# Optimization experiments

Hardware: AMD Instinct MI355X
Metric: run time of the kernel (lower is better)

## Reference

```python
import jax, jax.numpy as jnp
import numpy as np

D_MODEL = 1024
N_HEADS = 16
HEAD_DIM = D_MODEL // N_HEADS
D_FF = 4096
BATCH = 128
MEM_LEN = 1024
LN_EPS = 1e-5


def _layernorm(x, gamma, beta):
    mu = jnp.mean(x, axis=-1, keepdims=True)
    var = jnp.mean(jnp.square(x - mu), axis=-1, keepdims=True)
    return (x - mu) * jax.lax.rsqrt(var + LN_EPS) * gamma + beta


def setup_inputs() -> dict:
    key = jax.random.key(0)
    ks = jax.random.split(key, 12)
    s = 0.02
    return {
        "x": jax.random.normal(ks[0], (BATCH, D_MODEL), jnp.float32),
        "memory_keys": jax.random.normal(ks[1], (BATCH, MEM_LEN, D_MODEL), jnp.float32),
        "memory_values": jax.random.normal(ks[2], (BATCH, MEM_LEN, D_MODEL), jnp.float32),
        "alibi_bias": jax.random.normal(ks[3], (N_HEADS, 1, MEM_LEN), jnp.float32),
        "Wq": jax.random.normal(ks[4], (D_MODEL, D_MODEL), jnp.float32) * s,
        "bq": jnp.zeros((D_MODEL,), jnp.float32),
        "Wo": jax.random.normal(ks[5], (D_MODEL, D_MODEL), jnp.float32) * s,
        "bo": jnp.zeros((D_MODEL,), jnp.float32),
        "W1": jax.random.normal(ks[6], (D_MODEL, D_FF), jnp.float32) * s,
        "b1": jnp.zeros((D_FF,), jnp.float32),
        "W2": jax.random.normal(ks[7], (D_FF, D_MODEL), jnp.float32) * s,
        "b2": jnp.zeros((D_MODEL,), jnp.float32),
        "g1": jnp.ones((D_MODEL,), jnp.float32),
        "be1": jnp.zeros((D_MODEL,), jnp.float32),
        "g2": jnp.ones((D_MODEL,), jnp.float32),
        "be2": jnp.zeros((D_MODEL,), jnp.float32),
    }


def reference(x, memory_keys, memory_values, alibi_bias,
              Wq, bq, Wo, bo, W1, b1, W2, b2, g1, be1, g2, be2):
    B = x.shape[0]
    M = memory_keys.shape[1]
    # Q projection for the single query position: (B, H, hd)
    q = (x @ Wq + bq).reshape(B, N_HEADS, HEAD_DIM)
    k = memory_keys.reshape(B, M, N_HEADS, HEAD_DIM)
    v = memory_values.reshape(B, M, N_HEADS, HEAD_DIM)
    scale = 1.0 / np.sqrt(HEAD_DIM).astype(np.float32)
    # scores: (B, H, M) = q . k + ALiBi bias (broadcast over batch)
    scores = jnp.einsum("bhd,bmhd->bhm", q, k) * scale + alibi_bias[:, 0, :][None]
    attn = jax.nn.softmax(scores, axis=-1)
    attn_out = jnp.einsum("bhm,bmhd->bhd", attn, v).reshape(B, D_MODEL)
    attn_out = attn_out @ Wo + bo
    # residual + norm1 (dropout disabled in eval mode)
    h = _layernorm(x + attn_out, g1, be1)
    ff = jax.nn.relu(h @ W1 + b1) @ W2 + b2
    return _layernorm(h + ff, g2, be2)
```

## Files before the change

kernel.cpp:

```cpp
#include <hip/hip_runtime.h>
#include <hip/hip_bf16.h>
#include <math.h>

#define BATCH   128
#define DMODEL  1024
#define NHEADS  16
#define HEADDIM 64
#define DFF     4096
#define MEMLEN  1024
#define SPLIT   8
#define CHUNK   (MEMLEN / SPLIT)
#define QSPLIT  8
#define F1SPLIT 4
#define F2SPLIT 16

typedef __attribute__((ext_vector_type(8))) __bf16 bf16x8;
typedef __attribute__((ext_vector_type(4))) __bf16 bf16x4;
typedef __attribute__((ext_vector_type(4))) float  f32x4;

template<int ABF16, int KCHUNK>
__global__ __launch_bounds__(256) void gemm_k(
    const float* __restrict__ Af, const __bf16* __restrict__ Ab,
    const float* __restrict__ W, const float* __restrict__ bias,
    float* __restrict__ C, int N, int K)
{
    const int t    = threadIdx.x;
    const int lane = t & 63;
    const int w    = t >> 6;
    const int n0   = blockIdx.x * 64;
    const int m0   = blockIdx.y * 64;
    const int z    = blockIdx.z;
    const int kbeg = z * KCHUNK;

    __shared__ __bf16 As[2][64 * 56];
    __shared__ __bf16 Bs[2][64 * 56];

    const int ar = t >> 2, ac = (t & 3) * 8;
    const int bn = t & 63, bk = w * 8;
    const int q = lane >> 4, l15 = lane & 15;
    constexpr int ITERS = KCHUNK / 32;

    f32x4 acc[4] = {f32x4{0,0,0,0}, f32x4{0,0,0,0}, f32x4{0,0,0,0}, f32x4{0,0,0,0}};

    const float* wB   = W + (size_t)(kbeg + bk) * N + n0 + bn;
    const size_t aOff = (size_t)(m0 + ar) * K + kbeg + ac;

    {
        bf16x8 av;
        if constexpr (ABF16) {
            av = *(const bf16x8*)(Ab + aOff);
        } else {
            const float* ap = Af + aOff;
            float4 a0 = *(const float4*)ap, a1 = *(const float4*)(ap + 4);
            av[0]=(__bf16)a0.x; av[1]=(__bf16)a0.y; av[2]=(__bf16)a0.z; av[3]=(__bf16)a0.w;
            av[4]=(__bf16)a1.x; av[5]=(__bf16)a1.y; av[6]=(__bf16)a1.z; av[7]=(__bf16)a1.w;
        }
        bf16x8 bv;
        #pragma unroll
        for (int j = 0; j < 8; j++) bv[j] = (__bf16)wB[(size_t)j * N];
        *(bf16x8*)&As[0][ar * 56 + ac] = av;
        *(bf16x8*)&Bs[0][bn * 56 + bk] = bv;
    }
    __syncthreads();

    int cur = 0;
    #pragma unroll
    for (int it = 1; it < ITERS; ++it) {
        bf16x8 avn;
        float ax[8];
        if constexpr (ABF16) {
            avn = *(const bf16x8*)(Ab + aOff + it * 32);
        } else {
            const float* ap = Af + aOff + it * 32;
            float4 a0 = *(const float4*)ap, a1 = *(const float4*)(ap + 4);
            ax[0]=a0.x; ax[1]=a0.y; ax[2]=a0.z; ax[3]=a0.w;
            ax[4]=a1.x; ax[5]=a1.y; ax[6]=a1.z; ax[7]=a1.w;
        }
        float br[8];
        const float* wp = wB + (size_t)(it * 32) * N;
        #pragma unroll
        for (int j = 0; j < 8; j++) br[j] = wp[(size_t)j * N];

        bf16x8 af = *(const bf16x8*)&As[cur][(w * 16 + l15) * 56 + q * 8];
        #pragma unroll
        for (int c = 0; c < 4; c++) {
            bf16x8 bfv = *(const bf16x8*)&Bs[cur][(c * 16 + l15) * 56 + q * 8];
            acc[c] = __builtin_amdgcn_mfma_f32_16x16x32_bf16(af, bfv, acc[c], 0, 0, 0);
        }

        if constexpr (!ABF16) {
            #pragma unroll
            for (int j = 0; j < 8; j++) avn[j] = (__bf16)ax[j];
        }
        bf16x8 bvn;
        #pragma unroll
        for (int j = 0; j < 8; j++) bvn[j] = (__bf16)br[j];
        *(bf16x8*)&As[cur ^ 1][ar * 56 + ac] = avn;
        *(bf16x8*)&Bs[cur ^ 1][bn * 56 + bk] = bvn;
        __syncthreads();
        cur ^= 1;
    }

    {
        bf16x8 af = *(const bf16x8*)&As[cur][(w * 16 + l15) * 56 + q * 8];
        #pragma unroll
        for (int c = 0; c < 4; c++) {
            bf16x8 bfv = *(const bf16x8*)&Bs[cur][(c * 16 + l15) * 56 + q * 8];
            acc[c] = __builtin_amdgcn_mfma_f32_16x16x32_bf16(af, bfv, acc[c], 0, 0, 0);
        }
    }

    float* Cp = C + (size_t)z * ((size_t)BATCH * N);
    #pragma unroll
    for (int c = 0; c < 4; c++) {
        const int col = n0 + c * 16 + l15;
        const float bb = (z == 0) ? bias[col] : 0.0f;
        #pragma unroll
        for (int r = 0; r < 4; r++) {
            const int row = m0 + w * 16 + q * 4 + r;
            Cp[(size_t)row * N + col] = acc[c][r] + bb;
        }
    }
}

__global__ __launch_bounds__(256) void qsum_k(
    const float* __restrict__ qpart, float* __restrict__ qsum)
{
    const int b = blockIdx.x;
    const int t = threadIdx.x;
    const size_t idx = (size_t)b * DMODEL + 4 * t;
    float4 a = {0.f, 0.f, 0.f, 0.f};
    #pragma unroll
    for (int z = 0; z < QSPLIT; z++) {
        const float4 v = *(const float4*)&qpart[(size_t)z * (BATCH * DMODEL) + idx];
        a.x += v.x; a.y += v.y; a.z += v.z; a.w += v.w;
    }
    a.x *= 0.125f; a.y *= 0.125f; a.z *= 0.125f; a.w *= 0.125f;
    *(float4*)&qsum[idx] = a;
}

__global__ __launch_bounds__(256) void attn_partial_k(
    const float* __restrict__ qsum, const float* __restrict__ Kd,
    const float* __restrict__ Vd, const float* __restrict__ alibi,
    float* __restrict__ pacc, float* __restrict__ pl)
{
    const int s = blockIdx.x;
    const int b = blockIdx.y;
    const int t = threadIdx.x;
    const int h = t >> 4;

    const float4 qv = *(const float4*)&qsum[(size_t)b * DMODEL + 4 * t];
    float  l   = 0.0f;
    f32x4  acc = {0.f, 0.f, 0.f, 0.f};

    const size_t base = (size_t)b * MEMLEN * DMODEL + 4 * t;
    const float* __restrict__ ali = alibi + (size_t)h * MEMLEN + s * CHUNK;
    const size_t off0 = base + (size_t)(s * CHUNK) * DMODEL;

    #pragma unroll 4
    for (int i = 0; i < CHUNK; i++) {
        const size_t off = off0 + (size_t)i * DMODEL;
        const float4 kv = *(const float4*)&Kd[off];
        const float4 vv = *(const float4*)&Vd[off];
        float d = kv.x * qv.x + kv.y * qv.y + kv.z * qv.z + kv.w * qv.w;
        d += __shfl_xor(d, 1);
        d += __shfl_xor(d, 2);
        d += __shfl_xor(d, 4);
        d += __shfl_xor(d, 8);
        const float pw = __expf(d + ali[i]);
        l += pw;
        acc.x += pw * vv.x;
        acc.y += pw * vv.y;
        acc.z += pw * vv.z;
        acc.w += pw * vv.w;
    }
    *(f32x4*)&pacc[((size_t)(b * SPLIT + s)) * DMODEL + 4 * t] = acc;
    if ((t & 15) == 0) pl[(b * SPLIT + s) * NHEADS + h] = l;
}

__global__ __launch_bounds__(256) void attn_combine_k(
    const float* __restrict__ pacc, const float* __restrict__ pl,
    __bf16* __restrict__ attnb)
{
    const int b = blockIdx.x;
    const int t = threadIdx.x;
    const int h = t >> 4;

    float  L   = 0.0f;
    float4 acc = {0.f, 0.f, 0.f, 0.f};
    #pragma unroll
    for (int s = 0; s < SPLIT; s++) {
        L += pl[(b * SPLIT + s) * NHEADS + h];
        const float4 pa = *(const float4*)
            &pacc[((size_t)(b * SPLIT + s)) * DMODEL + 4 * t];
        acc.x += pa.x; acc.y += pa.y; acc.z += pa.z; acc.w += pa.w;
    }
    const float inv = 1.0f / L;
    bf16x4 o;
    o[0] = (__bf16)(acc.x * inv); o[1] = (__bf16)(acc.y * inv);
    o[2] = (__bf16)(acc.z * inv); o[3] = (__bf16)(acc.w * inv);
    *(bf16x4*)&attnb[(size_t)b * DMODEL + 4 * t] = o;
}

template<int NPARTS, bool WRITE_BF16>
__global__ __launch_bounds__(256) void ln_k(
    const float* __restrict__ xres, const float* __restrict__ parts,
    const float* __restrict__ g, const float* __restrict__ be,
    float* __restrict__ of32, __bf16* __restrict__ obf)
{
    const int b = blockIdx.x;
    const int t = threadIdx.x;
    float4 sv = *(const float4*)&xres[(size_t)b * DMODEL + 4 * t];
    #pragma unroll
    for (int z = 0; z < NPARTS; z++) {
        const float4 yv = *(const float4*)
            &parts[(size_t)z * (BATCH * DMODEL) + (size_t)b * DMODEL + 4 * t];
        sv.x += yv.x; sv.y += yv.y; sv.z += yv.z; sv.w += yv.w;
    }
    float sum = sv.x + sv.y + sv.z + sv.w;
    float sq  = sv.x * sv.x + sv.y * sv.y + sv.z * sv.z + sv.w * sv.w;
    #pragma unroll
    for (int mask = 1; mask < 64; mask <<= 1) {
        sum += __shfl_xor(sum, mask);
        sq  += __shfl_xor(sq, mask);
    }
    __shared__ float red[8];
    const int w = t >> 6;
    if ((t & 63) == 0) { red[w * 2] = sum; red[w * 2 + 1] = sq; }
    __syncthreads();
    sum = red[0] + red[2] + red[4] + red[6];
    sq  = red[1] + red[3] + red[5] + red[7];

    const float mu  = sum * (1.0f / DMODEL);
    const float var = sq * (1.0f / DMODEL) - mu * mu;
    const float rs  = rsqrtf(var + 1e-5f);

    const float4 gv  = *(const float4*)&g[4 * t];
    const float4 bev = *(const float4*)&be[4 * t];
    float4 o;
    o.x = (sv.x - mu) * rs * gv.x + bev.x;
    o.y = (sv.y - mu) * rs * gv.y + bev.y;
    o.z = (sv.z - mu) * rs * gv.z + bev.z;
    o.w = (sv.w - mu) * rs * gv.w + bev.w;
    *(float4*)&of32[(size_t)b * DMODEL + 4 * t] = o;
    if constexpr (WRITE_BF16) {
        bf16x4 ob;
        ob[0] = (__bf16)o.x; ob[1] = (__bf16)o.y;
        ob[2] = (__bf16)o.z; ob[3] = (__bf16)o.w;
        *(bf16x4*)&obf[(size_t)b * DMODEL + 4 * t] = ob;
    }
}

__global__ __launch_bounds__(256) void ff1reduce_k(
    const float* __restrict__ ffbpart, __bf16* __restrict__ ff1act)
{
    const int t = threadIdx.x;
    const size_t base = (size_t)blockIdx.x * 2048 + t * 8;
    float4 s0 = {0.f, 0.f, 0.f, 0.f}, s1 = {0.f, 0.f, 0.f, 0.f};
    #pragma unroll
    for (int z = 0; z < F1SPLIT; z++) {
        const float* pp = ffbpart + (size_t)z * ((size_t)BATCH * DFF) + base;
        const float4 a  = *(const float4*)pp;
        const float4 b4 = *(const float4*)(pp + 4);
        s0.x += a.x;  s0.y += a.y;  s0.z += a.z;  s0.w += a.w;
        s1.x += b4.x; s1.y += b4.y; s1.z += b4.z; s1.w += b4.w;
    }
    bf16x8 o;
    o[0] = (__bf16)fmaxf(s0.x, 0.f); o[1] = (__bf16)fmaxf(s0.y, 0.f);
    o[2] = (__bf16)fmaxf(s0.z, 0.f); o[3] = (__bf16)fmaxf(s0.w, 0.f);
    o[4] = (__bf16)fmaxf(s1.x, 0.f); o[5] = (__bf16)fmaxf(s1.y, 0.f);
    o[6] = (__bf16)fmaxf(s1.z, 0.f); o[7] = (__bf16)fmaxf(s1.w, 0.f);
    *(bf16x8*)&ff1act[base] = o;
}

extern "C" void kernel_launch(void* const* d_in, const int* in_sizes, int n_in,
                              void* d_out, int out_size, void* d_ws, size_t ws_size,
                              hipStream_t stream)
{
    const float* x   = (const float*)d_in[0];
    const float* mk  = (const float*)d_in[1];
    const float* mv  = (const float*)d_in[2];
    const float* ab  = (const float*)d_in[3];
    const float* Wq  = (const float*)d_in[4];
    const float* bq  = (const float*)d_in[5];
    const float* Wo  = (const float*)d_in[6];
    const float* bo  = (const float*)d_in[7];
    const float* W1  = (const float*)d_in[8];
    const float* b1  = (const float*)d_in[9];
    const float* W2  = (const float*)d_in[10];
    const float* b2  = (const float*)d_in[11];
    const float* g1  = (const float*)d_in[12];
    const float* be1 = (const float*)d_in[13];
    const float* g2  = (const float*)d_in[14];
    const float* be2 = (const float*)d_in[15];
    float* out = (float*)d_out;

    float* wsf      = (float*)d_ws;
    float* qpart    = wsf;
    float* qsum     = wsf + 1048576;
    float* tmppart  = wsf + 1179648;
    float* hbuf     = wsf + 2228224;
    float* ffbpart  = wsf + 2359296;
    float* tmp2part = wsf + 4456448;
    float* pacc     = wsf + 6553600;
    float* pl       = wsf + 7602176;
    __bf16* attnb   = (__bf16*)(wsf + 7618560);
    __bf16* hbf     = (__bf16*)(wsf + 7684096);
    __bf16* ff1act  = (__bf16*)(wsf + 7749632);

    gemm_k<0, DMODEL / QSPLIT><<<dim3(16, 2, QSPLIT), 256, 0, stream>>>(
        x, nullptr, Wq, bq, qpart, DMODEL, DMODEL);
    qsum_k<<<BATCH, 256, 0, stream>>>(qpart, qsum);
    attn_partial_k<<<dim3(SPLIT, BATCH), 256, 0, stream>>>(
        qsum, mk, mv, ab, pacc, pl);
    attn_combine_k<<<BATCH, 256, 0, stream>>>(pacc, pl, attnb);
    gemm_k<1, DMODEL / QSPLIT><<<dim3(16, 2, QSPLIT), 256, 0, stream>>>(
        nullptr, attnb, Wo, bo, tmppart, DMODEL, DMODEL);
    ln_k<QSPLIT, true><<<BATCH, 256, 0, stream>>>(
        x, tmppart, g1, be1, hbuf, hbf);
    gemm_k<1, DMODEL / F1SPLIT><<<dim3(64, 2, F1SPLIT), 256, 0, stream>>>(
        nullptr, hbf, W1, b1, ffbpart, DFF, DMODEL);
    ff1reduce_k<<<(BATCH * DFF) / 2048, 256, 0, stream>>>(ffbpart, ff1act);
    gemm_k<1, DFF / F2SPLIT><<<dim3(16, 2, F2SPLIT), 256, 0, stream>>>(
        nullptr, ff1act, W2, b2, tmp2part, DMODEL, DFF);
    ln_k<F2SPLIT, false><<<BATCH, 256, 0, stream>>>(
        hbuf, tmp2part, g2, be2, out, nullptr);
}
```

Baseline: 1.055 ms.

## Fuse split-K reductions into consumer kernels and retune split factors

Removes the separate qsum and ff1reduce kernels. The attention partial kernel now sums the Q split-K partials itself, and the W2 GEMM sums two FF1 partials and applies ReLU while loading its A operand. Split factors are retuned: attention memory split doubled, and the Q, FF1 and FF2 K-splits halved. The GEMM loop count becomes a runtime value instead of a compile-time unrolled constant, which may cost some scheduling quality. Each attention block re-reads the Q partials redundantly, and FF2 reads fp32 inputs instead of bf16.

After: 1.071 ms. Within noise of the previous version (+1.5%).

```diff
diff --git a/kernel.cpp b/kernel.cpp
--- a/kernel.cpp
+++ b/kernel.cpp
@@ -8,21 +8,22 @@
 #define HEADDIM 64
 #define DFF     4096
 #define MEMLEN  1024
-#define SPLIT   8
+#define SPLIT   16
 #define CHUNK   (MEMLEN / SPLIT)
-#define QSPLIT  8
-#define F1SPLIT 4
-#define F2SPLIT 16
+#define QSPLIT  4
+#define F1SPLIT 2
+#define F2SPLIT 8
 
 typedef __attribute__((ext_vector_type(8))) __bf16 bf16x8;
 typedef __attribute__((ext_vector_type(4))) __bf16 bf16x4;
 typedef __attribute__((ext_vector_type(4))) float  f32x4;
 
-template<int ABF16, int KCHUNK>
+template<int ABF16, int APARTS, int RELU>
 __global__ __launch_bounds__(256) void gemm_k(
-    const float* __restrict__ Af, const __bf16* __restrict__ Ab,
+    const float* __restrict__ Af, size_t aPartStride,
+    const __bf16* __restrict__ Ab,
     const float* __restrict__ W, const float* __restrict__ bias,
-    float* __restrict__ C, int N, int K)
+    float* __restrict__ C, int N, int K, int kchunk)
 {
     const int t    = threadIdx.x;
     const int lane = t & 63;
@@ -30,7 +31,7 @@
     const int n0   = blockIdx.x * 64;
     const int m0   = blockIdx.y * 64;
     const int z    = blockIdx.z;
-    const int kbeg = z * KCHUNK;
+    const int kbeg = z * kchunk;
 
     __shared__ __bf16 As[2][64 * 56];
     __shared__ __bf16 Bs[2][64 * 56];
@@ -38,7 +39,6 @@
     const int ar = t >> 2, ac = (t & 3) * 8;
     const int bn = t & 63, bk = w * 8;
     const int q = lane >> 4, l15 = lane & 15;
-    constexpr int ITERS = KCHUNK / 32;
 
     f32x4 acc[4] = {f32x4{0,0,0,0}, f32x4{0,0,0,0}, f32x4{0,0,0,0}, f32x4{0,0,0,0}};
 
@@ -52,8 +52,19 @@
         } else {
             const float* ap = Af + aOff;
             float4 a0 = *(const float4*)ap, a1 = *(const float4*)(ap + 4);
-            av[0]=(__bf16)a0.x; av[1]=(__bf16)a0.y; av[2]=(__bf16)a0.z; av[3]=(__bf16)a0.w;
-            av[4]=(__bf16)a1.x; av[5]=(__bf16)a1.y; av[6]=(__bf16)a1.z; av[7]=(__bf16)a1.w;
+            float va[8] = {a0.x, a0.y, a0.z, a0.w, a1.x, a1.y, a1.z, a1.w};
+            if constexpr (APARTS == 2) {
+                const float* a2 = ap + aPartStride;
+                float4 y0 = *(const float4*)a2, y1 = *(const float4*)(a2 + 4);
+                va[0]+=y0.x; va[1]+=y0.y; va[2]+=y0.z; va[3]+=y0.w;
+                va[4]+=y1.x; va[5]+=y1.y; va[6]+=y1.z; va[7]+=y1.w;
+            }
+            #pragma unroll
+            for (int j = 0; j < 8; j++) {
+                float v = va[j];
+                if (RELU) v = fmaxf(v, 0.0f);
+                av[j] = (__bf16)v;
+            }
         }
         bf16x8 bv;
         #pragma unroll
@@ -63,9 +74,9 @@
     }
     __syncthreads();
 
+    const int iters = kchunk >> 5;
     int cur = 0;
-    #pragma unroll
-    for (int it = 1; it < ITERS; ++it) {
+    for (int it = 1; it < iters; ++it) {
         bf16x8 avn;
         float ax[8];
         if constexpr (ABF16) {
@@ -75,6 +86,12 @@
             float4 a0 = *(const float4*)ap, a1 = *(const float4*)(ap + 4);
             ax[0]=a0.x; ax[1]=a0.y; ax[2]=a0.z; ax[3]=a0.w;
             ax[4]=a1.x; ax[5]=a1.y; ax[6]=a1.z; ax[7]=a1.w;
+            if constexpr (APARTS == 2) {
+                const float* a2 = ap + aPartStride;
+                float4 y0 = *(const float4*)a2, y1 = *(const float4*)(a2 + 4);
+                ax[0]+=y0.x; ax[1]+=y0.y; ax[2]+=y0.z; ax[3]+=y0.w;
+                ax[4]+=y1.x; ax[5]+=y1.y; ax[6]+=y1.z; ax[7]+=y1.w;
+            }
         }
         float br[8];
         const float* wp = wB + (size_t)(it * 32) * N;
@@ -90,7 +107,11 @@
 
         if constexpr (!ABF16) {
             #pragma unroll
-            for (int j = 0; j < 8; j++) avn[j] = (__bf16)ax[j];
+            for (int j = 0; j < 8; j++) {
+                float v = ax[j];
+                if (RELU) v = fmaxf(v, 0.0f);
+                avn[j] = (__bf16)v;
+            }
         }
         bf16x8 bvn;
         #pragma unroll
@@ -123,24 +144,8 @@
     }
 }
 
-__global__ __launch_bounds__(256) void qsum_k(
-    const float* __restrict__ qpart, float* __restrict__ qsum)
-{
-    const int b = blockIdx.x;
-    const int t = threadIdx.x;
-    const size_t idx = (size_t)b * DMODEL + 4 * t;
-    float4 a = {0.f, 0.f, 0.f, 0.f};
-    #pragma unroll
-    for (int z = 0; z < QSPLIT; z++) {
-        const float4 v = *(const float4*)&qpart[(size_t)z * (BATCH * DMODEL) + idx];
-        a.x += v.x; a.y += v.y; a.z += v.z; a.w += v.w;
-    }
-    a.x *= 0.125f; a.y *= 0.125f; a.z *= 0.125f; a.w *= 0.125f;
-    *(float4*)&qsum[idx] = a;
-}
-
 __global__ __launch_bounds__(256) void attn_partial_k(
-    const float* __restrict__ qsum, const float* __restrict__ Kd,
+    const float* __restrict__ qpart, const float* __restrict__ Kd,
     const float* __restrict__ Vd, const float* __restrict__ alibi,
     float* __restrict__ pacc, float* __restrict__ pl)
 {
@@ -149,7 +154,16 @@
     const int t = threadIdx.x;
     const int h = t >> 4;
 
-    const float4 qv = *(const float4*)&qsum[(size_t)b * DMODEL + 4 * t];
+    float4 qv = {0.f, 0.f, 0.f, 0.f};
+    #pragma unroll
+    for (int z = 0; z < QSPLIT; z++) {
+        const float4 qp = *(const float4*)
+            &qpart[(size_t)z * (BATCH * DMODEL) + (size_t)b * DMODEL + 4 * t];
+        qv.x += qp.x; qv.y += qp.y; qv.z += qp.z; qv.w += qp.w;
+    }
+    const float scale = 0.125f;
+    qv.x *= scale; qv.y *= scale; qv.z *= scale; qv.w *= scale;
+
     float  l   = 0.0f;
     f32x4  acc = {0.f, 0.f, 0.f, 0.f};
 
@@ -249,28 +263,6 @@
         ob[2] = (__bf16)o.z; ob[3] = (__bf16)o.w;
         *(bf16x4*)&obf[(size_t)b * DMODEL + 4 * t] = ob;
     }
-}
-
-__global__ __launch_bounds__(256) void ff1reduce_k(
-    const float* __restrict__ ffbpart, __bf16* __restrict__ ff1act)
-{
-    const int t = threadIdx.x;
-    const size_t base = (size_t)blockIdx.x * 2048 + t * 8;
-    float4 s0 = {0.f, 0.f, 0.f, 0.f}, s1 = {0.f, 0.f, 0.f, 0.f};
-    #pragma unroll
-    for (int z = 0; z < F1SPLIT; z++) {
-        const float* pp = ffbpart + (size_t)z * ((size_t)BATCH * DFF) + base;
-        const float4 a  = *(const float4*)pp;
-        const float4 b4 = *(const float4*)(pp + 4);
-        s0.x += a.x;  s0.y += a.y;  s0.z += a.z;  s0.w += a.w;
-        s1.x += b4.x; s1.y += b4.y; s1.z += b4.z; s1.w += b4.w;
-    }
-    bf16x8 o;
-    o[0] = (__bf16)fmaxf(s0.x, 0.f); o[1] = (__bf16)fmaxf(s0.y, 0.f);
-    o[2] = (__bf16)fmaxf(s0.z, 0.f); o[3] = (__bf16)fmaxf(s0.w, 0.f);
-    o[4] = (__bf16)fmaxf(s1.x, 0.f); o[5] = (__bf16)fmaxf(s1.y, 0.f);
-    o[6] = (__bf16)fmaxf(s1.z, 0.f); o[7] = (__bf16)fmaxf(s1.w, 0.f);
-    *(bf16x8*)&ff1act[base] = o;
 }
 
 extern "C" void kernel_launch(void* const* d_in, const int* in_sizes, int n_in,
@@ -297,32 +289,29 @@
 
     float* wsf      = (float*)d_ws;
     float* qpart    = wsf;
-    float* qsum     = wsf + 1048576;
-    float* tmppart  = wsf + 1179648;
-    float* hbuf     = wsf + 2228224;
-    float* ffbpart  = wsf + 2359296;
-    float* tmp2part = wsf + 4456448;
-    float* pacc     = wsf + 6553600;
-    float* pl       = wsf + 7602176;
-    __bf16* attnb   = (__bf16*)(wsf + 7618560);
-    __bf16* hbf     = (__bf16*)(wsf + 7684096);
-    __bf16* ff1act  = (__bf16*)(wsf + 7749632);
-
-    gemm_k<0, DMODEL / QSPLIT><<<dim3(16, 2, QSPLIT), 256, 0, stream>>>(
-        x, nullptr, Wq, bq, qpart, DMODEL, DMODEL);
-    qsum_k<<<BATCH, 256, 0, stream>>>(qpart, qsum);
+    float* tmppart  = wsf + 524288;
+    float* hbuf     = wsf + 1048576;
+    float* ffbpart  = wsf + 1179648;
+    float* tmp2part = wsf + 2228224;
+    float* pacc     = wsf + 3276800;
+    float* pl       = wsf + 5373952;
+    __bf16* attnb   = (__bf16*)(wsf + 5406720);
+    __bf16* hbf     = (__bf16*)(wsf + 5472256);
+
+    gemm_k<0, 1, 0><<<dim3(16, 2, QSPLIT), 256, 0, stream>>>(
+        x, 0, nullptr, Wq, bq, qpart, DMODEL, DMODEL, DMODEL / QSPLIT);
     attn_partial_k<<<dim3(SPLIT, BATCH), 256, 0, stream>>>(
-        qsum, mk, mv, ab, pacc, pl);
+        qpart, mk, mv, ab, pacc, pl);
     attn_combine_k<<<BATCH, 256, 0, stream>>>(pacc, pl, attnb);
-    gemm_k<1, DMODEL / QSPLIT><<<dim3(16, 2, QSPLIT), 256, 0, stream>>>(
-        nullptr, attnb, Wo, bo, tmppart, DMODEL, DMODEL);
+    gemm_k<1, 1, 0><<<dim3(16, 2, QSPLIT), 256, 0, stream>>>(
+        nullptr, 0, attnb, Wo, bo, tmppart, DMODEL, DMODEL, DMODEL / QSPLIT);
     ln_k<QSPLIT, true><<<BATCH, 256, 0, stream>>>(
         x, tmppart, g1, be1, hbuf, hbf);
-    gemm_k<1, DMODEL / F1SPLIT><<<dim3(64, 2, F1SPLIT), 256, 0, stream>>>(
-        nullptr, hbf, W1, b1, ffbpart, DFF, DMODEL);
-    ff1reduce_k<<<(BATCH * DFF) / 2048, 256, 0, stream>>>(ffbpart, ff1act);
-    gemm_k<1, DFF / F2SPLIT><<<dim3(16, 2, F2SPLIT), 256, 0, stream>>>(
-        nullptr, ff1act, W2, b2, tmp2part, DMODEL, DFF);
+    gemm_k<1, 1, 0><<<dim3(64, 2, F1SPLIT), 256, 0, stream>>>(
+        nullptr, 0, hbf, W1, b1, ffbpart, DFF, DMODEL, DMODEL / F1SPLIT);
+    gemm_k<0, 2, 1><<<dim3(16, 2, F2SPLIT), 256, 0, stream>>>(
+        ffbpart, (size_t)BATCH * DFF, nullptr, W2, b2, tmp2part,
+        DMODEL, DFF, DFF / F2SPLIT);
     ln_k<F2SPLIT, false><<<BATCH, 256, 0, stream>>>(
         hbuf, tmp2part, g2, be2, out, nullptr);
 }
```
